# Kernel tuning notes

Measured on AMD Instinct MI355X. Metric: run time of the kernel, lower is better.

## Reference

```python
import jax, jax.numpy as jnp
import numpy as np

N, FIN, FOUT = 4096, 512, 256
ALPHA = 0.2          # LeakyReLU negative slope
NEG_INF = -9e15      # mask value from the torch source


def setup_inputs() -> dict:
    key = jax.random.key(0)
    ks = jax.random.split(key, 11)
    h = jax.random.normal(ks[0], (N, FIN), dtype=jnp.float32)
    adj_n = jax.random.randint(ks[1], (N, N), 0, 2, dtype=jnp.int32)
    adj_d = jax.random.randint(ks[2], (N, N), 0, 2, dtype=jnp.int32)
    G_nd = jax.random.normal(ks[3], (2, N, FOUT), dtype=jnp.float32)
    # learned parameters (xavier-ish scale)
    W_n = jax.random.normal(ks[4], (FIN, FOUT), dtype=jnp.float32) * 0.05
    a1_n = jax.random.normal(ks[5], (FOUT, 1), dtype=jnp.float32) * 0.05
    a2_n = jax.random.normal(ks[6], (FOUT, 1), dtype=jnp.float32) * 0.05
    W_d = jax.random.normal(ks[7], (FIN, FOUT), dtype=jnp.float32) * 0.05
    a1_d = jax.random.normal(ks[8], (FOUT, 1), dtype=jnp.float32) * 0.05
    a2_d = jax.random.normal(ks[9], (FOUT, 1), dtype=jnp.float32) * 0.05
    scale = jnp.zeros((1,), dtype=jnp.float32)
    return {"h": h, "adj_n": adj_n, "adj_d": adj_d, "G_nd": G_nd,
            "W_n": W_n, "a1_n": a1_n, "a2_n": a2_n,
            "W_d": W_d, "a1_d": a1_d, "a2_d": a2_d, "scale": scale}


def _gat(h, adj, W, a1, a2):
    # Wh: [N, FOUT]
    Wh = h @ W
    # outer-sum attention logits: e[i,j] = leakyrelu(Wh_i.a1 + Wh_j.a2)
    e = jax.nn.leaky_relu((Wh @ a1) + (Wh @ a2).T, negative_slope=ALPHA)  # [N, N]
    att = jnp.where(adj > 0, e, jnp.float32(NEG_INF))
    att = jax.nn.softmax(att, axis=-1)
    # dropout is identity in eval mode
    return jax.nn.elu(att @ Wh)  # [N, FOUT]


def reference(h, adj_n, adj_d, G_nd, W_n, a1_n, a2_n, W_d, a1_d, a2_d, scale):
    f_n_S = _gat(h, adj_n, W_n, a1_n, a2_n)
    f_d_S = _gat(h, adj_d, W_d, a1_d, a2_d)
    # The G_nd cross-attention branch (f_nd_C) in the torch source is computed
    # but never used in the returned value; omitted here (jit would DCE it).
    return f_n_S + f_d_S
```

## Files before the change

### kernel.cpp

```cpp
#include <hip/hip_runtime.h>

#define N_NODES 4096
#define FIN     512
#define FOUT    256
#define NSPLIT  4
#define NTILES  ((N_NODES / NSPLIT) / 64)

typedef __attribute__((ext_vector_type(8))) short bf16x8s;
typedef __attribute__((ext_vector_type(4))) float f32x4;
typedef __attribute__((ext_vector_type(8))) unsigned short u16x8;
typedef unsigned short u16;
typedef unsigned int   u32;

__device__ inline u16 f2b(float f) {
    union { float f; unsigned int u; } v; v.f = f;
    unsigned int r = v.u + 0x7fffu + ((v.u >> 16) & 1u);
    return (u16)(r >> 16);
}

__global__ __launch_bounds__(256) void prep_kernel(
    const float* __restrict__ h, const float* __restrict__ Wn,
    const float* __restrict__ Wd,
    u16* __restrict__ hb, u16* __restrict__ WTb, float* __restrict__ s12)
{
    __shared__ u16 tl[64 * 72];
    const int t = threadIdx.x;
    const int bid = blockIdx.x;

    if (bid < 1024) {
        int idx = (bid * 256 + t) * 8;
        float4 f0 = *(const float4*)&h[idx];
        float4 f1 = *(const float4*)&h[idx + 4];
        u16x8 o;
        o[0]=f2b(f0.x); o[1]=f2b(f0.y); o[2]=f2b(f0.z); o[3]=f2b(f0.w);
        o[4]=f2b(f1.x); o[5]=f2b(f1.y); o[6]=f2b(f1.z); o[7]=f2b(f1.w);
        *(u16x8*)&hb[idx] = o;
    } else if (bid < 1088) {
        int id = bid - 1024;
        int kx = id & 7, ny = (id >> 3) & 3, b = id >> 5;
        const float* W = b ? Wd : Wn;
        int k0 = kx * 64, n0 = ny * 64;
        int kr = t >> 2, nc0 = (t & 3) * 16;
        const float* src = W + (size_t)(k0 + kr) * FOUT + n0 + nc0;
        #pragma unroll
        for (int jv = 0; jv < 4; ++jv) {
            float4 f = *(const float4*)(src + jv * 4);
            tl[(nc0 + jv * 4 + 0) * 72 + kr] = f2b(f.x);
            tl[(nc0 + jv * 4 + 1) * 72 + kr] = f2b(f.y);
            tl[(nc0 + jv * 4 + 2) * 72 + kr] = f2b(f.z);
            tl[(nc0 + jv * 4 + 3) * 72 + kr] = f2b(f.w);
        }
        __syncthreads();
        int n = t >> 2, kc0 = (t & 3) * 16;
        u16* dst = WTb + ((size_t)b << 17) + (size_t)(n0 + n) * FIN + k0 + kc0;
        *(uint4*)dst       = *(uint4*)&tl[n * 72 + kc0];
        *(uint4*)(dst + 8) = *(uint4*)&tl[n * 72 + kc0 + 8];
    } else {
        float4 z = {0.f, 0.f, 0.f, 0.f};
        float4* p4 = (float4*)s12;
        #pragma unroll
        for (int k = 0; k < 16; ++k) p4[k * 256 + t] = z;
    }
}

__global__ __launch_bounds__(256) void wh_gemm_kernel(
    const u16* __restrict__ hb, const u16* __restrict__ WTb,
    const float* __restrict__ a1n, const float* __restrict__ a2n,
    const float* __restrict__ a1d, const float* __restrict__ a2d,
    u16* __restrict__ WhT, float* __restrict__ s1, float* __restrict__ s2)
{
    __shared__ u16 smem[8192];
    u16* a_lds = smem;
    u16* b_lds = smem + 4096;

    const int t = threadIdx.x, lane = t & 63, w = t >> 6;
    const int q = lane >> 4, ln = lane & 15;
    const int i0 = blockIdx.x * 64, n0 = blockIdx.y * 64, b = blockIdx.z;
    const u16* wt = WTb + ((size_t)b << 17);

    f32x4 acc[4];
    #pragma unroll
    for (int i = 0; i < 4; ++i) acc[i] = (f32x4){0.f, 0.f, 0.f, 0.f};

    for (int kt = 0; kt < 8; ++kt) {
        const int k0 = kt * 64;
        __syncthreads();
        #pragma unroll
        for (int it = 0; it < 2; ++it) {
            int chunk = it * 256 + t;
            int r = chunk >> 3, kc = chunk & 7;
            const u16* g = hb + (size_t)(i0 + r) * FIN + k0 + ((kc ^ (r & 7)) * 8);
            u16* l = a_lds + (it * 256 + w * 64) * 8;
            __builtin_amdgcn_global_load_lds(
                (const __attribute__((address_space(1))) void*)g,
                (__attribute__((address_space(3))) void*)l, 16, 0, 0);
        }
        #pragma unroll
        for (int it = 0; it < 2; ++it) {
            int chunk = it * 256 + t;
            int n = chunk >> 3, kc = chunk & 7;
            const u16* g = wt + (size_t)(n0 + n) * FIN + k0 + ((kc ^ (n & 7)) * 8);
            u16* l = b_lds + (it * 256 + w * 64) * 8;
            __builtin_amdgcn_global_load_lds(
                (const __attribute__((address_space(1))) void*)g,
                (__attribute__((address_space(3))) void*)l, 16, 0, 0);
        }
        __syncthreads();
        #pragma unroll
        for (int ks = 0; ks < 2; ++ks) {
            int sw = ((ks * 4 + q) ^ (ln & 7)) * 8;
            bf16x8s af = *(const bf16x8s*)&a_lds[(w * 16 + ln) * 64 + sw];
            #pragma unroll
            for (int nt = 0; nt < 4; ++nt) {
                bf16x8s bfv = *(const bf16x8s*)&b_lds[(nt * 16 + ln) * 64 + sw];
                acc[nt] = __builtin_amdgcn_mfma_f32_16x16x32_bf16(af, bfv, acc[nt], 0, 0, 0);
            }
        }
    }

    {
        const float* a1 = b ? a1d : a1n;
        const float* a2 = b ? a2d : a2n;
        float s1p[4] = {0.f, 0.f, 0.f, 0.f};
        float s2p[4] = {0.f, 0.f, 0.f, 0.f};
        #pragma unroll
        for (int nt = 0; nt < 4; ++nt) {
            float va1 = a1[n0 + nt * 16 + ln];
            float va2 = a2[n0 + nt * 16 + ln];
            #pragma unroll
            for (int r = 0; r < 4; ++r) {
                s1p[r] += acc[nt][r] * va1;
                s2p[r] += acc[nt][r] * va2;
            }
        }
        #pragma unroll
        for (int r = 0; r < 4; ++r) {
            #pragma unroll
            for (int off = 8; off >= 1; off >>= 1) {
                s1p[r] += __shfl_xor(s1p[r], off);
                s2p[r] += __shfl_xor(s2p[r], off);
            }
            if (ln == 0) {
                int row = i0 + w * 16 + q * 4 + r;
                atomicAdd(&s1[b * N_NODES + row], s1p[r]);
                atomicAdd(&s2[b * N_NODES + row], s2p[r]);
            }
        }
    }

    __syncthreads();
    #pragma unroll
    for (int nt = 0; nt < 4; ++nt)
        #pragma unroll
        for (int r = 0; r < 4; ++r)
            smem[(nt * 16 + ln) * 72 + (w * 16 + q * 4 + r)] = f2b(acc[nt][r]);
    __syncthreads();
    {
        const int nl = t >> 2, is = (t & 3) * 16;
        u16* dst = WhT + ((size_t)b << 20) + (size_t)(n0 + nl) * N_NODES + i0 + is;
        *(uint4*)dst       = *(uint4*)&smem[nl * 72 + is];
        *(uint4*)(dst + 8) = *(uint4*)&smem[nl * 72 + is + 8];
    }
}

__global__ __launch_bounds__(256) void attn_kernel(
    const int* __restrict__ adj_n, const int* __restrict__ adj_d,
    const u16* __restrict__ WhT,
    const float* __restrict__ s1, const float* __restrict__ s2,
    float* __restrict__ num_ws, float* __restrict__ den_ws)
{
    __shared__ u16 wht_lds[256 * 64];
    __shared__ u16 p_lds[64 * 64];
    __shared__ float den_lds[64];

    const int t = threadIdx.x, lane = t & 63, w = t >> 6;
    const int q = lane >> 4, ln = lane & 15;
    const int b = blockIdx.z, split = blockIdx.y;
    const int i0 = blockIdx.x * 64;

    const int* adjb = b ? adj_d : adj_n;
    const u16* whtB = WhT + ((size_t)b << 20);
    const float* s1b = s1 + b * N_NODES;
    const float* s2b = s2 + b * N_NODES;

    const int pr = t >> 3;
    const int cw = t & 7;
    const int pc = cw * 8;
    const float s1v0 = s1b[i0 + pr];
    const float s1v1 = s1b[i0 + pr + 32];
    const size_t arow0 = (size_t)(i0 + pr) * N_NODES + pc;
    const size_t arow1 = arow0 + (size_t)32 * N_NODES;

    if (t < 64) den_lds[t] = 0.f;

    f32x4 acc[4][4];
    #pragma unroll
    for (int mt = 0; mt < 4; ++mt)
        #pragma unroll
        for (int nt = 0; nt < 4; ++nt) acc[mt][nt] = (f32x4){0.f, 0.f, 0.f, 0.f};

    const int jbase = split * (N_NODES / NSPLIT);
    int4 a00_pf = *(const int4*)&adjb[arow0 + jbase];
    int4 a01_pf = *(const int4*)&adjb[arow0 + jbase + 4];
    int4 a10_pf = *(const int4*)&adjb[arow1 + jbase];
    int4 a11_pf = *(const int4*)&adjb[arow1 + jbase + 4];
    float4 sv0_pf = *(const float4*)&s2b[jbase + pc];
    float4 sv1_pf = *(const float4*)&s2b[jbase + pc + 4];

    for (int jt = 0; jt < NTILES; ++jt) {
        const int j0 = jbase + jt * 64;
        __syncthreads();
        #pragma unroll
        for (int it = 0; it < 8; ++it) {
            int chunk = it * 256 + t;
            int n = chunk >> 3, kc = chunk & 7;
            const u16* g = whtB + (size_t)n * N_NODES + j0 + ((kc ^ (n & 7)) * 8);
            u16* l = wht_lds + (it * 256 + w * 64) * 8;
            __builtin_amdgcn_global_load_lds(
                (const __attribute__((address_space(1))) void*)g,
                (__attribute__((address_space(3))) void*)l, 16, 0, 0);
        }
        int4 a00 = a00_pf, a01 = a01_pf, a10 = a10_pf, a11 = a11_pf;
        float4 sv0 = sv0_pf, sv1 = sv1_pf;
        if (jt < NTILES - 1) {
            const int jn = j0 + 64;
            a00_pf = *(const int4*)&adjb[arow0 + jn];
            a01_pf = *(const int4*)&adjb[arow0 + jn + 4];
            a10_pf = *(const int4*)&adjb[arow1 + jn];
            a11_pf = *(const int4*)&adjb[arow1 + jn + 4];
            sv0_pf = *(const float4*)&s2b[jn + pc];
            sv1_pf = *(const float4*)&s2b[jn + pc + 4];
        }
        int v0[8] = {a00.x, a00.y, a00.z, a00.w, a01.x, a01.y, a01.z, a01.w};
        int v1[8] = {a10.x, a10.y, a10.z, a10.w, a11.x, a11.y, a11.z, a11.w};
        float svf[8] = {sv0.x, sv0.y, sv0.z, sv0.w, sv1.x, sv1.y, sv1.z, sv1.w};
        float d0 = 0.f, d1 = 0.f;
        u16x8 pk0, pk1;
        #pragma unroll
        for (int jj = 0; jj < 8; ++jj) {
            float sv = svf[jj];
            float x0 = s1v0 + sv, x1 = s1v1 + sv;
            float p0 = (v0[jj] > 0) ? __expf(fmaxf(x0, 0.2f * x0)) : 0.f;
            float p1 = (v1[jj] > 0) ? __expf(fmaxf(x1, 0.2f * x1)) : 0.f;
            d0 += p0; d1 += p1;
            pk0[jj] = f2b(p0); pk1[jj] = f2b(p1);
        }
        d0 += __shfl_down(d0, 4, 8); d1 += __shfl_down(d1, 4, 8);
        d0 += __shfl_down(d0, 2, 8); d1 += __shfl_down(d1, 2, 8);
        d0 += __shfl_down(d0, 1, 8); d1 += __shfl_down(d1, 1, 8);
        if ((t & 7) == 0) { den_lds[pr] += d0; den_lds[pr + 32] += d1; }
        int swp = ((cw ^ (pr & 7)) * 8);
        *(u16x8*)&p_lds[pr * 64 + swp] = pk0;
        *(u16x8*)&p_lds[(pr + 32) * 64 + swp] = pk1;
        __syncthreads();
        #pragma unroll
        for (int ks = 0; ks < 2; ++ks) {
            int sw = ((ks * 4 + q) ^ (ln & 7)) * 8;
            bf16x8s af[4];
            #pragma unroll
            for (int mt = 0; mt < 4; ++mt)
                af[mt] = *(const bf16x8s*)&p_lds[(mt * 16 + ln) * 64 + sw];
            #pragma unroll
            for (int nt = 0; nt < 4; ++nt) {
                bf16x8s bfv = *(const bf16x8s*)&wht_lds[(w * 64 + nt * 16 + ln) * 64 + sw];
                #pragma unroll
                for (int mt = 0; mt < 4; ++mt)
                    acc[mt][nt] = __builtin_amdgcn_mfma_f32_16x16x32_bf16(af[mt], bfv, acc[mt][nt], 0, 0, 0);
            }
        }
    }
    const size_t pbase = (size_t)(b * NSPLIT + split) * N_NODES;
    #pragma unroll
    for (int mt = 0; mt < 4; ++mt)
        #pragma unroll
        for (int r = 0; r < 4; ++r) {
            int row = mt * 16 + q * 4 + r;
            #pragma unroll
            for (int nt = 0; nt < 4; ++nt)
                num_ws[(pbase + i0 + row) * FOUT + w * 64 + nt * 16 + ln] = acc[mt][nt][r];
        }
    if (t < 64) den_ws[pbase + i0 + t] = den_lds[t];
}

__global__ __launch_bounds__(256) void reduce_kernel(
    const float* __restrict__ num_ws, const float* __restrict__ den_ws,
    float* __restrict__ out)
{
    int gid = blockIdx.x * 256 + threadIdx.x;
    int i = gid >> 6;
    int f4 = (gid & 63) * 4;
    float4 o = {0.f, 0.f, 0.f, 0.f};
    #pragma unroll
    for (int b = 0; b < 2; ++b) {
        float4 num = {0.f, 0.f, 0.f, 0.f};
        float den = 0.f;
        #pragma unroll
        for (int s = 0; s < NSPLIT; ++s) {
            const float4 v = *(const float4*)&num_ws[((size_t)(b * NSPLIT + s) * N_NODES + i) * FOUT + f4];
            num.x += v.x; num.y += v.y; num.z += v.z; num.w += v.w;
            den += den_ws[(size_t)(b * NSPLIT + s) * N_NODES + i];
        }
        float inv = 1.0f / den;
        float e0 = num.x * inv, e1 = num.y * inv, e2 = num.z * inv, e3 = num.w * inv;
        o.x += (e0 > 0.f) ? e0 : expm1f(e0);
        o.y += (e1 > 0.f) ? e1 : expm1f(e1);
        o.z += (e2 > 0.f) ? e2 : expm1f(e2);
        o.w += (e3 > 0.f) ? e3 : expm1f(e3);
    }
    *(float4*)&out[(size_t)i * FOUT + f4] = o;
}

extern "C" void kernel_launch(void* const* d_in, const int* in_sizes, int n_in,
                              void* d_out, int out_size, void* d_ws, size_t ws_size,
                              hipStream_t stream) {
    const float* h    = (const float*)d_in[0];
    const int*   adjn = (const int*)d_in[1];
    const int*   adjd = (const int*)d_in[2];
    const float* Wn   = (const float*)d_in[4];
    const float* a1n  = (const float*)d_in[5];
    const float* a2n  = (const float*)d_in[6];
    const float* Wd   = (const float*)d_in[7];
    const float* a1d  = (const float*)d_in[8];
    const float* a2d  = (const float*)d_in[9];

    char* ws = (char*)d_ws;
    u16*  WhT  = (u16*)ws;
    float* s1  = (float*)(ws + ((size_t)8 << 20));
    float* s2  = s1 + 2 * N_NODES;
    float* den = s2 + 2 * N_NODES;
    u16*  hb   = (u16*)(ws + ((size_t)8 << 20) + ((size_t)256 << 10));
    u16*  WTb  = (u16*)(ws + ((size_t)12 << 20) + ((size_t)256 << 10));
    float* num = (float*)(ws + ((size_t)8 << 20) + ((size_t)256 << 10));

    prep_kernel<<<1089, 256, 0, stream>>>(h, Wn, Wd, hb, WTb, s1);
    wh_gemm_kernel<<<dim3(64, 4, 2), 256, 0, stream>>>(hb, WTb, a1n, a2n, a1d, a2d, WhT, s1, s2);
    attn_kernel<<<dim3(64, NSPLIT, 2), 256, 0, stream>>>(adjn, adjd, WhT, s1, s2, num, den);
    reduce_kernel<<<1024, 256, 0, stream>>>(num, den, (float*)d_out);
}
```

Before: 212.7 us.

## Double-buffer WhT LDS tiles with async prefetch and relaxed waitcnt barriers

The WhT tile buffer in LDS is doubled. The next tile's global_load_lds is issued before the current tile's softmax and MFMA work, so memory latency overlaps compute. The full __syncthreads is replaced by a manual s_waitcnt vmcnt(14) plus s_barrier with sched barriers, and setprio is raised around the MFMA block. The per-row denominators now accumulate in registers instead of LDS atomics-free adds. The cost is roughly doubled LDS use, which may lower occupancy, and a hand-tuned vmcnt that relies on load issue order.

After: 211.5 us. No clear change (-0.6%).

```diff
diff --git a/kernel.cpp b/kernel.cpp
--- a/kernel.cpp
+++ b/kernel.cpp
@@ -169,9 +169,8 @@
     const float* __restrict__ s1, const float* __restrict__ s2,
     float* __restrict__ num_ws, float* __restrict__ den_ws)
 {
-    __shared__ u16 wht_lds[256 * 64];
+    __shared__ u16 wht_lds[2][256 * 64];
     __shared__ u16 p_lds[64 * 64];
-    __shared__ float den_lds[64];
 
     const int t = threadIdx.x, lane = t & 63, w = t >> 6;
     const int q = lane >> 4, ln = lane & 15;
@@ -191,7 +190,7 @@
     const size_t arow0 = (size_t)(i0 + pr) * N_NODES + pc;
     const size_t arow1 = arow0 + (size_t)32 * N_NODES;
 
-    if (t < 64) den_lds[t] = 0.f;
+    float den0 = 0.f, den1 = 0.f;
 
     f32x4 acc[4][4];
     #pragma unroll
@@ -200,6 +199,17 @@
         for (int nt = 0; nt < 4; ++nt) acc[mt][nt] = (f32x4){0.f, 0.f, 0.f, 0.f};
 
     const int jbase = split * (N_NODES / NSPLIT);
+
+    #pragma unroll
+    for (int it = 0; it < 8; ++it) {
+        int chunk = it * 256 + t;
+        int n = chunk >> 3, kc = chunk & 7;
+        const u16* g = whtB + (size_t)n * N_NODES + jbase + ((kc ^ (n & 7)) * 8);
+        u16* l = &wht_lds[0][(it * 256 + w * 64) * 8];
+        __builtin_amdgcn_global_load_lds(
+            (const __attribute__((address_space(1))) void*)g,
+            (__attribute__((address_space(3))) void*)l, 16, 0, 0);
+    }
     int4 a00_pf = *(const int4*)&adjb[arow0 + jbase];
     int4 a01_pf = *(const int4*)&adjb[arow0 + jbase + 4];
     int4 a10_pf = *(const int4*)&adjb[arow1 + jbase];
@@ -208,17 +218,21 @@
     float4 sv1_pf = *(const float4*)&s2b[jbase + pc + 4];
 
     for (int jt = 0; jt < NTILES; ++jt) {
+        const int cur = jt & 1, nxt = cur ^ 1;
         const int j0 = jbase + jt * 64;
-        __syncthreads();
-        #pragma unroll
-        for (int it = 0; it < 8; ++it) {
-            int chunk = it * 256 + t;
-            int n = chunk >> 3, kc = chunk & 7;
-            const u16* g = whtB + (size_t)n * N_NODES + j0 + ((kc ^ (n & 7)) * 8);
-            u16* l = wht_lds + (it * 256 + w * 64) * 8;
-            __builtin_amdgcn_global_load_lds(
-                (const __attribute__((address_space(1))) void*)g,
-                (__attribute__((address_space(3))) void*)l, 16, 0, 0);
+
+        if (jt < NTILES - 1) {
+            const int jn = j0 + 64;
+            #pragma unroll
+            for (int it = 0; it < 8; ++it) {
+                int chunk = it * 256 + t;
+                int n = chunk >> 3, kc = chunk & 7;
+                const u16* g = whtB + (size_t)n * N_NODES + jn + ((kc ^ (n & 7)) * 8);
+                u16* l = &wht_lds[nxt][(it * 256 + w * 64) * 8];
+                __builtin_amdgcn_global_load_lds(
+                    (const __attribute__((address_space(1))) void*)g,
+                    (__attribute__((address_space(3))) void*)l, 16, 0, 0);
+            }
         }
         int4 a00 = a00_pf, a01 = a01_pf, a10 = a10_pf, a11 = a11_pf;
         float4 sv0 = sv0_pf, sv1 = sv1_pf;
@@ -248,11 +262,17 @@
         d0 += __shfl_down(d0, 4, 8); d1 += __shfl_down(d1, 4, 8);
         d0 += __shfl_down(d0, 2, 8); d1 += __shfl_down(d1, 2, 8);
         d0 += __shfl_down(d0, 1, 8); d1 += __shfl_down(d1, 1, 8);
-        if ((t & 7) == 0) { den_lds[pr] += d0; den_lds[pr + 32] += d1; }
+        if ((t & 7) == 0) { den0 += d0; den1 += d1; }
         int swp = ((cw ^ (pr & 7)) * 8);
         *(u16x8*)&p_lds[pr * 64 + swp] = pk0;
         *(u16x8*)&p_lds[(pr + 32) * 64 + swp] = pk1;
-        __syncthreads();
+
+        __builtin_amdgcn_sched_barrier(0);
+        asm volatile("s_waitcnt vmcnt(14) lgkmcnt(0)" ::: "memory");
+        __builtin_amdgcn_s_barrier();
+        __builtin_amdgcn_sched_barrier(0);
+
+        __builtin_amdgcn_s_setprio(1);
         #pragma unroll
         for (int ks = 0; ks < 2; ++ks) {
             int sw = ((ks * 4 + q) ^ (ln & 7)) * 8;
@@ -262,12 +282,17 @@
                 af[mt] = *(const bf16x8s*)&p_lds[(mt * 16 + ln) * 64 + sw];
             #pragma unroll
             for (int nt = 0; nt < 4; ++nt) {
-                bf16x8s bfv = *(const bf16x8s*)&wht_lds[(w * 64 + nt * 16 + ln) * 64 + sw];
+                bf16x8s bfv = *(const bf16x8s*)&wht_lds[cur][(w * 64 + nt * 16 + ln) * 64 + sw];
                 #pragma unroll
                 for (int mt = 0; mt < 4; ++mt)
                     acc[mt][nt] = __builtin_amdgcn_mfma_f32_16x16x32_bf16(af[mt], bfv, acc[mt][nt], 0, 0, 0);
             }
         }
+        __builtin_amdgcn_s_setprio(0);
+
+        __builtin_amdgcn_sched_barrier(0);
+        __builtin_amdgcn_s_barrier();
+        __builtin_amdgcn_sched_barrier(0);
     }
     const size_t pbase = (size_t)(b * NSPLIT + split) * N_NODES;
     #pragma unroll
@@ -279,7 +304,10 @@
             for (int nt = 0; nt < 4; ++nt)
                 num_ws[(pbase + i0 + row) * FOUT + w * 64 + nt * 16 + ln] = acc[mt][nt][r];
         }
-    if (t < 64) den_ws[pbase + i0 + t] = den_lds[t];
+    if ((t & 7) == 0) {
+        den_ws[pbase + i0 + pr] = den0;
+        den_ws[pbase + i0 + pr + 32] = den1;
+    }
 }
 
 __global__ __launch_bounds__(256) void reduce_kernel(
```

## Double-buffer WhT and P tiles in LDS to overlap loads with MFMA

Applied to the files above, without the earlier changes.

Converts the attention kernel's main loop to a double-buffered software pipeline. The WhT tile load and the P computation for the next tile are issued before the MFMA on the current tile, leaving one barrier per iteration instead of two. Denominator accumulation moves from shared-memory read-modify-write to per-thread registers that are written once at the end. LDS use doubles to roughly 80KB per block, which may lower occupancy.

Result: no change. 216.0 us (+1.6%).

```diff
diff --git a/kernel.cpp b/kernel.cpp
--- a/kernel.cpp
+++ b/kernel.cpp
@@ -169,9 +169,8 @@
     const float* __restrict__ s1, const float* __restrict__ s2,
     float* __restrict__ num_ws, float* __restrict__ den_ws)
 {
-    __shared__ u16 wht_lds[256 * 64];
-    __shared__ u16 p_lds[64 * 64];
-    __shared__ float den_lds[64];
+    __shared__ u16 wht_lds[2][256 * 64];
+    __shared__ u16 p_lds[2][64 * 64];
 
     const int t = threadIdx.x, lane = t & 63, w = t >> 6;
     const int q = lane >> 4, ln = lane & 15;
@@ -190,8 +189,9 @@
     const float s1v1 = s1b[i0 + pr + 32];
     const size_t arow0 = (size_t)(i0 + pr) * N_NODES + pc;
     const size_t arow1 = arow0 + (size_t)32 * N_NODES;
-
-    if (t < 64) den_lds[t] = 0.f;
+    const int swp = (cw ^ (pr & 7)) * 8;
+
+    float den0 = 0.f, den1 = 0.f;
 
     f32x4 acc[4][4];
     #pragma unroll
@@ -200,75 +200,103 @@
         for (int nt = 0; nt < 4; ++nt) acc[mt][nt] = (f32x4){0.f, 0.f, 0.f, 0.f};
 
     const int jbase = split * (N_NODES / NSPLIT);
-    int4 a00_pf = *(const int4*)&adjb[arow0 + jbase];
-    int4 a01_pf = *(const int4*)&adjb[arow0 + jbase + 4];
-    int4 a10_pf = *(const int4*)&adjb[arow1 + jbase];
-    int4 a11_pf = *(const int4*)&adjb[arow1 + jbase + 4];
-    float4 sv0_pf = *(const float4*)&s2b[jbase + pc];
-    float4 sv1_pf = *(const float4*)&s2b[jbase + pc + 4];
-
-    for (int jt = 0; jt < NTILES; ++jt) {
-        const int j0 = jbase + jt * 64;
+
+#define STAGE_WHT(BUF, J0) do {                                               \
+    _Pragma("unroll")                                                         \
+    for (int it_ = 0; it_ < 8; ++it_) {                                       \
+        int chunk_ = it_ * 256 + t;                                           \
+        int n_ = chunk_ >> 3, kc_ = chunk_ & 7;                               \
+        const u16* g_ = whtB + (size_t)n_ * N_NODES + (J0) + ((kc_ ^ (n_ & 7)) * 8); \
+        u16* l_ = &wht_lds[BUF][(it_ * 256 + w * 64) * 8];                    \
+        __builtin_amdgcn_global_load_lds(                                     \
+            (const __attribute__((address_space(1))) void*)g_,                \
+            (__attribute__((address_space(3))) void*)l_, 16, 0, 0);           \
+    } } while (0)
+
+#define P_COMPUTE(BUF, A00, A01, A10, A11, SV0, SV1) do {                     \
+    int v0_[8] = {(A00).x, (A00).y, (A00).z, (A00).w,                         \
+                  (A01).x, (A01).y, (A01).z, (A01).w};                        \
+    int v1_[8] = {(A10).x, (A10).y, (A10).z, (A10).w,                         \
+                  (A11).x, (A11).y, (A11).z, (A11).w};                        \
+    float sv_[8] = {(SV0).x, (SV0).y, (SV0).z, (SV0).w,                       \
+                    (SV1).x, (SV1).y, (SV1).z, (SV1).w};                      \
+    float d0_ = 0.f, d1_ = 0.f;                                               \
+    u16x8 pk0_, pk1_;                                                         \
+    _Pragma("unroll")                                                         \
+    for (int jj_ = 0; jj_ < 8; ++jj_) {                                       \
+        float sv_j = sv_[jj_];                                                \
+        float x0_ = s1v0 + sv_j, x1_ = s1v1 + sv_j;                           \
+        float p0_ = (v0_[jj_] > 0) ? __expf(fmaxf(x0_, 0.2f * x0_)) : 0.f;    \
+        float p1_ = (v1_[jj_] > 0) ? __expf(fmaxf(x1_, 0.2f * x1_)) : 0.f;    \
+        d0_ += p0_; d1_ += p1_;                                               \
+        pk0_[jj_] = f2b(p0_); pk1_[jj_] = f2b(p1_);                           \
+    }                                                                         \
+    d0_ += __shfl_down(d0_, 4, 8); d1_ += __shfl_down(d1_, 4, 8);             \
+    d0_ += __shfl_down(d0_, 2, 8); d1_ += __shfl_down(d1_, 2, 8);             \
+    d0_ += __shfl_down(d0_, 1, 8); d1_ += __shfl_down(d1_, 1, 8);             \
+    den0 += d0_; den1 += d1_;                                                 \
+    *(u16x8*)&p_lds[BUF][pr * 64 + swp] = pk0_;                               \
+    *(u16x8*)&p_lds[BUF][(pr + 32) * 64 + swp] = pk1_;                        \
+} while (0)
+
+#define MFMA_TILE(BUF) do {                                                   \
+    _Pragma("unroll")                                                         \
+    for (int ks_ = 0; ks_ < 2; ++ks_) {                                       \
+        int sw_ = ((ks_ * 4 + q) ^ (ln & 7)) * 8;                             \
+        bf16x8s af0_ = *(const bf16x8s*)&p_lds[BUF][(0 * 16 + ln) * 64 + sw_];\
+        bf16x8s af1_ = *(const bf16x8s*)&p_lds[BUF][(1 * 16 + ln) * 64 + sw_];\
+        bf16x8s af2_ = *(const bf16x8s*)&p_lds[BUF][(2 * 16 + ln) * 64 + sw_];\
+        bf16x8s af3_ = *(const bf16x8s*)&p_lds[BUF][(3 * 16 + ln) * 64 + sw_];\
+        _Pragma("unroll")                                                     \
+        for (int nt_ = 0; nt_ < 4; ++nt_) {                                   \
+            bf16x8s bfv_ = *(const bf16x8s*)&wht_lds[BUF][(w * 64 + nt_ * 16 + ln) * 64 + sw_]; \
+            acc[0][nt_] = __builtin_amdgcn_mfma_f32_16x16x32_bf16(af0_, bfv_, acc[0][nt_], 0, 0, 0); \
+            acc[1][nt_] = __builtin_amdgcn_mfma_f32_16x16x32_bf16(af1_, bfv_, acc[1][nt_], 0, 0, 0); \
+            acc[2][nt_] = __builtin_amdgcn_mfma_f32_16x16x32_bf16(af2_, bfv_, acc[2][nt_], 0, 0, 0); \
+            acc[3][nt_] = __builtin_amdgcn_mfma_f32_16x16x32_bf16(af3_, bfv_, acc[3][nt_], 0, 0, 0); \
+        }                                                                     \
+    } } while (0)
+
+    STAGE_WHT(0, jbase);
+    int4 c00 = *(const int4*)&adjb[arow0 + jbase];
+    int4 c01 = *(const int4*)&adjb[arow0 + jbase + 4];
+    int4 c10 = *(const int4*)&adjb[arow1 + jbase];
+    int4 c11 = *(const int4*)&adjb[arow1 + jbase + 4];
+    float4 cs0 = *(const float4*)&s2b[jbase + pc];
+    float4 cs1 = *(const float4*)&s2b[jbase + pc + 4];
+    int4 a00_pf = *(const int4*)&adjb[arow0 + jbase + 64];
+    int4 a01_pf = *(const int4*)&adjb[arow0 + jbase + 64 + 4];
+    int4 a10_pf = *(const int4*)&adjb[arow1 + jbase + 64];
+    int4 a11_pf = *(const int4*)&adjb[arow1 + jbase + 64 + 4];
+    float4 sv0_pf = *(const float4*)&s2b[jbase + 64 + pc];
+    float4 sv1_pf = *(const float4*)&s2b[jbase + 64 + pc + 4];
+    P_COMPUTE(0, c00, c01, c10, c11, cs0, cs1);
+    __syncthreads();
+
+    for (int jt = 0; jt < NTILES - 1; ++jt) {
+        const int cur = jt & 1, nxt = cur ^ 1;
+        STAGE_WHT(nxt, jbase + (jt + 1) * 64);
+        c00 = a00_pf; c01 = a01_pf; c10 = a10_pf; c11 = a11_pf;
+        cs0 = sv0_pf; cs1 = sv1_pf;
+        {
+            const int j2 = jbase + ((jt + 2 < NTILES) ? jt + 2 : NTILES - 1) * 64;
+            a00_pf = *(const int4*)&adjb[arow0 + j2];
+            a01_pf = *(const int4*)&adjb[arow0 + j2 + 4];
+            a10_pf = *(const int4*)&adjb[arow1 + j2];
+            a11_pf = *(const int4*)&adjb[arow1 + j2 + 4];
+            sv0_pf = *(const float4*)&s2b[j2 + pc];
+            sv1_pf = *(const float4*)&s2b[j2 + pc + 4];
+        }
+        P_COMPUTE(nxt, c00, c01, c10, c11, cs0, cs1);
+        MFMA_TILE(cur);
         __syncthreads();
-        #pragma unroll
-        for (int it = 0; it < 8; ++it) {
-            int chunk = it * 256 + t;
-            int n = chunk >> 3, kc = chunk & 7;
-            const u16* g = whtB + (size_t)n * N_NODES + j0 + ((kc ^ (n & 7)) * 8);
-            u16* l = wht_lds + (it * 256 + w * 64) * 8;
-            __builtin_amdgcn_global_load_lds(
-                (const __attribute__((address_space(1))) void*)g,
-                (__attribute__((address_space(3))) void*)l, 16, 0, 0);
-        }
-        int4 a00 = a00_pf, a01 = a01_pf, a10 = a10_pf, a11 = a11_pf;
-        float4 sv0 = sv0_pf, sv1 = sv1_pf;
-        if (jt < NTILES - 1) {
-            const int jn = j0 + 64;
-            a00_pf = *(const int4*)&adjb[arow0 + jn];
-            a01_pf = *(const int4*)&adjb[arow0 + jn + 4];
-            a10_pf = *(const int4*)&adjb[arow1 + jn];
-            a11_pf = *(const int4*)&adjb[arow1 + jn + 4];
-            sv0_pf = *(const float4*)&s2b[jn + pc];
-            sv1_pf = *(const float4*)&s2b[jn + pc + 4];
-        }
-        int v0[8] = {a00.x, a00.y, a00.z, a00.w, a01.x, a01.y, a01.z, a01.w};
-        int v1[8] = {a10.x, a10.y, a10.z, a10.w, a11.x, a11.y, a11.z, a11.w};
-        float svf[8] = {sv0.x, sv0.y, sv0.z, sv0.w, sv1.x, sv1.y, sv1.z, sv1.w};
-        float d0 = 0.f, d1 = 0.f;
-        u16x8 pk0, pk1;
-        #pragma unroll
-        for (int jj = 0; jj < 8; ++jj) {
-            float sv = svf[jj];
-            float x0 = s1v0 + sv, x1 = s1v1 + sv;
-            float p0 = (v0[jj] > 0) ? __expf(fmaxf(x0, 0.2f * x0)) : 0.f;
-            float p1 = (v1[jj] > 0) ? __expf(fmaxf(x1, 0.2f * x1)) : 0.f;
-            d0 += p0; d1 += p1;
-            pk0[jj] = f2b(p0); pk1[jj] = f2b(p1);
-        }
-        d0 += __shfl_down(d0, 4, 8); d1 += __shfl_down(d1, 4, 8);
-        d0 += __shfl_down(d0, 2, 8); d1 += __shfl_down(d1, 2, 8);
-        d0 += __shfl_down(d0, 1, 8); d1 += __shfl_down(d1, 1, 8);
-        if ((t & 7) == 0) { den_lds[pr] += d0; den_lds[pr + 32] += d1; }
-        int swp = ((cw ^ (pr & 7)) * 8);
-        *(u16x8*)&p_lds[pr * 64 + swp] = pk0;
-        *(u16x8*)&p_lds[(pr + 32) * 64 + swp] = pk1;
-        __syncthreads();
-        #pragma unroll
-        for (int ks = 0; ks < 2; ++ks) {
-            int sw = ((ks * 4 + q) ^ (ln & 7)) * 8;
-            bf16x8s af[4];
-            #pragma unroll
-            for (int mt = 0; mt < 4; ++mt)
-                af[mt] = *(const bf16x8s*)&p_lds[(mt * 16 + ln) * 64 + sw];
-            #pragma unroll
-            for (int nt = 0; nt < 4; ++nt) {
-                bf16x8s bfv = *(const bf16x8s*)&wht_lds[(w * 64 + nt * 16 + ln) * 64 + sw];
-                #pragma unroll
-                for (int mt = 0; mt < 4; ++mt)
-                    acc[mt][nt] = __builtin_amdgcn_mfma_f32_16x16x32_bf16(af[mt], bfv, acc[mt][nt], 0, 0, 0);
-            }
-        }
-    }
+    }
+    MFMA_TILE((NTILES - 1) & 1);
+
+#undef STAGE_WHT
+#undef P_COMPUTE
+#undef MFMA_TILE
+
     const size_t pbase = (size_t)(b * NSPLIT + split) * N_NODES;
     #pragma unroll
     for (int mt = 0; mt < 4; ++mt)
@@ -279,7 +307,10 @@
             for (int nt = 0; nt < 4; ++nt)
                 num_ws[(pbase + i0 + row) * FOUT + w * 64 + nt * 16 + ln] = acc[mt][nt][r];
         }
-    if (t < 64) den_ws[pbase + i0 + t] = den_lds[t];
+    if ((t & 7) == 0) {
+        den_ws[pbase + i0 + pr] = den0;
+        den_ws[pbase + i0 + pr + 32] = den1;
+    }
 }
 
 __global__ __launch_bounds__(256) void reduce_kernel(
```
